# Kernel tuning notes

Measured on AMD Instinct MI355X. Metric: run time of the kernel, lower is better.

The kernel has to match this reference:

```python
import jax, jax.numpy as jnp
from jax import lax
import numpy as np

B, TQ, T = 64, 2, 2048
HID, ENC, U, FILT, K = 1024, 512, 256, 32, 31


def setup_inputs() -> dict:
    key = jax.random.key(0)
    ks = jax.random.split(key, 12)
    def w(k, shape, fan_in):
        return jax.random.normal(k, shape, jnp.float32) / np.sqrt(fan_in)
    return {
        "query": jax.random.normal(ks[0], (B, TQ, HID), jnp.float32),
        "state": jax.random.uniform(ks[1], (B, T), jnp.float32),
        "memory": jax.random.normal(ks[2], (B, T, ENC), jnp.float32),
        "Wq": w(ks[3], (HID, U), HID), "bq": jnp.zeros((U,), jnp.float32),
        "Wm": w(ks[4], (ENC, U), ENC), "bm": jnp.zeros((U,), jnp.float32),
        "Wl": w(ks[5], (FILT, U), FILT), "bl": jnp.zeros((U,), jnp.float32),
        "conv_w": w(ks[6], (FILT, 1, K), K), "conv_b": jnp.zeros((FILT,), jnp.float32),
        "We": w(ks[7], (U, U), U), "be": jnp.zeros((U,), jnp.float32),
        "v_a": w(ks[8], (U,), U),
    }


def reference(query, state, memory, Wq, bq, Wm, bm, Wl, bl, conv_w, conv_b, We, be, v_a):
    # memory projection (done in `initialize` in the original): [B,T,U]
    mem_proj = jnp.einsum("bte,eu->btu", memory, Wm) + bm
    # query projection then slice timestep 1 -> [B,1,U]
    pq = (jnp.einsum("bqh,hu->bqu", query, Wq) + bq)[:, 1:2, :]
    # location features: 1-D conv over time of previous alignment, 'same' padding
    x = state[:, None, :]                                    # [B,1,T]
    f = lax.conv_general_dilated(x, conv_w, (1,), "SAME",
                                 dimension_numbers=("NCH", "OIH", "NCH"))
    f = f + conv_b[None, :, None]                            # [B,FILT,T]
    loc = jnp.einsum("bft,fu->btu", f, Wl) + bl              # [B,T,U]
    # additive energy with tanh, reduced against v_a -> [B,T]
    h = jnp.tanh(jnp.einsum("btu,uv->btv", pq + loc + mem_proj, We) + be)
    energy = jnp.einsum("btu,u->bt", h, v_a)
    # smoothing normalization: sigmoid / sum(sigmoid)
    s = jax.nn.sigmoid(energy)
    alignment = s / jnp.sum(s, axis=-1, keepdims=True)
    # cumulate_weights=True: accumulate onto previous alignment
    cum_alignment = state + alignment
    # context against projected memory: [B,1,U]
    context = jnp.einsum("bt,btu->bu", cum_alignment, mem_proj)[:, None, :]
    return context
```

## Files before the change

### kernel.cpp

```cpp
#include <hip/hip_runtime.h>
#include <hip/hip_bf16.h>
#include <math.h>

#define Bq 64
#define Tt 2048
#define TQn 2
#define HIDn 1024
#define ENCn 512
#define Un 256
#define FILTn 32
#define KKn 31

#define TTILE 32
#define NCHUNK (Tt / TTILE)
#define LDK 520

typedef short short8 __attribute__((ext_vector_type(8)));
typedef float f32x4  __attribute__((ext_vector_type(4)));
typedef float f32x4v __attribute__((ext_vector_type(4)));
typedef unsigned short ushort_t;
typedef unsigned int   uint_t;

union S8 { short8 v; uint_t u[4]; };

__device__ __forceinline__ ushort_t f2b(float f) {
    union { float f; uint_t u; } x; x.f = f;
    uint_t r = x.u + 0x7fffu + ((x.u >> 16) & 1u);
    return (ushort_t)(r >> 16);
}
__device__ __forceinline__ uint_t cvt_pk(float lo, float hi) {
    union { __hip_bfloat162 h; uint_t u; } x;
    x.h = __float22bfloat162_rn(make_float2(lo, hi));
    return x.u;
}
__device__ __forceinline__ float b2f(uint_t u16) {
    union { uint_t i; float f; } x; x.i = u16 << 16;
    return x.f;
}
__device__ __forceinline__ float tanh_fast(float x) {
    const float e = __expf(2.0f * x);
    return 1.0f - 2.0f * __builtin_amdgcn_rcpf(e + 1.0f);
}

__device__ __forceinline__ int bp_idx(int v, int k) {
    const int seg = (k >> 5) * 16 + (v >> 6) * 4 + ((v >> 4) & 3);
    const int ln  = ((k >> 3) & 3) * 16 + (v & 15);
    return seg * 512 + ln * 8 + (k & 7);
}

__global__ void k_prep(const float* __restrict__ We, const float* __restrict__ Wm,
                       const float* __restrict__ Wl, const float* __restrict__ conv_w,
                       const float* __restrict__ bq, const float* __restrict__ bm,
                       const float* __restrict__ bl, const float* __restrict__ conv_b,
                       const float* __restrict__ query, const float* __restrict__ Wq,
                       const float* __restrict__ be,
                       ushort_t* __restrict__ Bp, ushort_t* __restrict__ CWT,
                       float* __restrict__ zconst)
{
    const int blk = blockIdx.x;
    __shared__ float wlwe[FILTn * 64];
    __shared__ float g_lds[Un];
    if (blk < 512) {
        const int v = threadIdx.x;
        const int e = blk;
        float a0 = 0.f, a1 = 0.f, a2 = 0.f, a3 = 0.f;
        #pragma unroll 4
        for (int u = 0; u < Un; u += 4) {
            a0 += Wm[(size_t)e * Un + u + 0] * We[(u + 0) * Un + v];
            a1 += Wm[(size_t)e * Un + u + 1] * We[(u + 1) * Un + v];
            a2 += Wm[(size_t)e * Un + u + 2] * We[(u + 2) * Un + v];
            a3 += Wm[(size_t)e * Un + u + 3] * We[(u + 3) * Un + v];
        }
        Bp[bp_idx(v, e)] = f2b((a0 + a1) + (a2 + a3));
    } else if (blk < 516) {
        const int vc = (blk - 512) * 64;
        for (int i = threadIdx.x; i < FILTn * 64; i += 256) {
            const int f = i >> 6, vv = i & 63;
            float a = 0.f;
            #pragma unroll 8
            for (int u = 0; u < Un; ++u) a += Wl[f * Un + u] * We[u * Un + vc + vv];
            wlwe[f * 64 + vv] = a;
        }
        __syncthreads();
        for (int i = threadIdx.x; i < 64 * 32; i += 256) {
            const int vv = i >> 5, k = i & 31;
            float a = 0.f;
            if (k < KKn) {
                #pragma unroll
                for (int f = 0; f < FILTn; ++f) a += conv_w[f * KKn + k] * wlwe[f * 64 + vv];
            }
            CWT[bp_idx(vc + vv, k)] = f2b(a);
        }
    } else {
        const int b = blk - 516;
        const int u = threadIdx.x;
        float cv = bq[u] + bm[u] + bl[u];
        #pragma unroll
        for (int f = 0; f < FILTn; ++f) cv += conv_b[f] * Wl[f * Un + u];
        const float* q = query + ((size_t)b * TQn + 1) * HIDn;
        float a0 = 0.f, a1 = 0.f, a2 = 0.f, a3 = 0.f;
        #pragma unroll 4
        for (int h = 0; h < HIDn; h += 4) {
            a0 += q[h + 0] * Wq[(size_t)(h + 0) * Un + u];
            a1 += q[h + 1] * Wq[(size_t)(h + 1) * Un + u];
            a2 += q[h + 2] * Wq[(size_t)(h + 2) * Un + u];
            a3 += q[h + 3] * Wq[(size_t)(h + 3) * Un + u];
        }
        g_lds[u] = cv + (a0 + a1) + (a2 + a3);
        __syncthreads();
        float z0 = 0.f, z1 = 0.f;
        #pragma unroll 4
        for (int uu = 0; uu < Un; uu += 2) {
            z0 += g_lds[uu]     * We[(size_t)uu * Un + u];
            z1 += g_lds[uu + 1] * We[(size_t)(uu + 1) * Un + u];
        }
        zconst[b * Un + u] = be[u] + z0 + z1;
    }
}

__global__ __launch_bounds__(256, 4) void attn_main(
    const float* __restrict__ memory, const float* __restrict__ state,
    const ushort_t* __restrict__ Bp, const ushort_t* __restrict__ CWT,
    const float* __restrict__ zconst, const float* __restrict__ v_a,
    float* __restrict__ zA, float* __restrict__ zS,
    float* __restrict__ zSsum, float* __restrict__ zStsum)
{
    const int blk = blockIdx.x;
    const int b  = blk >> 6;
    const int c  = blk & (NCHUNK - 1);
    const int t0 = c * TTILE;
    const int tid = threadIdx.x;

    __shared__ __align__(16) ushort_t mem_s[TTILE * LDK];
    __shared__ __align__(16) float sw_raw[80];
    __shared__ __align__(16) float ep_s[4][TTILE];
    __shared__ __align__(16) float s_s[TTILE];
    float* sw = sw_raw + 1;

    for (int i = tid; i < TTILE + 31; i += 256) {
        const int t = t0 - 15 + i;
        sw[i] = (t >= 0 && t < Tt) ? state[b * Tt + t] : 0.0f;
    }

    const int lane = tid & 63;
    const int w    = tid >> 6;
    const int lm   = lane & 15;
    const int lq   = lane >> 4;
    const int ncol0 = w * 64 + lm;

    const ushort_t* bp0 = Bp + (size_t)(w * 4) * 512 + lane * 8;
    const ushort_t* bp1 = bp0 + 512;
    const ushort_t* bp2 = bp0 + 1024;
    const ushort_t* bp3 = bp0 + 1536;
    const ushort_t* cp0 = CWT + (size_t)(w * 4) * 512 + lane * 8;

    short8 bbuf[2][4];
    bbuf[0][0] = *(const short8*)(bp0);
    bbuf[0][1] = *(const short8*)(bp1);
    bbuf[0][2] = *(const short8*)(bp2);
    bbuf[0][3] = *(const short8*)(bp3);
    bbuf[1][0] = *(const short8*)(bp0 + 8192);
    bbuf[1][1] = *(const short8*)(bp1 + 8192);
    bbuf[1][2] = *(const short8*)(bp2 + 8192);
    bbuf[1][3] = *(const short8*)(bp3 + 8192);

    const f32x4v* memv4 = (const f32x4v*)(memory + ((size_t)b * Tt + t0) * ENCn);
    #pragma unroll
    for (int i = 0; i < 8; ++i) {
        const int idx = i * 256 + tid;
        const int row = idx >> 6;
        const int cw8 = (idx & 63) << 3;
        const f32x4v m0 = __builtin_nontemporal_load(memv4 + 2 * idx);
        const f32x4v m1 = __builtin_nontemporal_load(memv4 + 2 * idx + 1);
        S8 v;
        v.u[0] = cvt_pk(m0.x, m0.y); v.u[1] = cvt_pk(m0.z, m0.w);
        v.u[2] = cvt_pk(m1.x, m1.y); v.u[3] = cvt_pk(m1.z, m1.w);
        *(short8*)&mem_s[row * LDK + cw8] = v.v;
    }

    f32x4 acc[2][4] = {};

    __syncthreads();

    const ushort_t* arow0 = &mem_s[(lm) * LDK + lq * 8];
    const ushort_t* arow1 = &mem_s[(16 + lm) * LDK + lq * 8];

    short8 a0c = *(const short8*)(arow0);
    short8 a1c = *(const short8*)(arow1);

    #pragma unroll
    for (int s = 0; s < 16; ++s) {
        const int sa = ((s + 1) & 15) * 32;
        const short8 a0n = *(const short8*)(arow0 + sa);
        const short8 a1n = *(const short8*)(arow1 + sa);
        acc[0][0] = __builtin_amdgcn_mfma_f32_16x16x32_bf16(a0c, bbuf[s & 1][0], acc[0][0], 0, 0, 0);
        acc[0][1] = __builtin_amdgcn_mfma_f32_16x16x32_bf16(a0c, bbuf[s & 1][1], acc[0][1], 0, 0, 0);
        acc[0][2] = __builtin_amdgcn_mfma_f32_16x16x32_bf16(a0c, bbuf[s & 1][2], acc[0][2], 0, 0, 0);
        acc[0][3] = __builtin_amdgcn_mfma_f32_16x16x32_bf16(a0c, bbuf[s & 1][3], acc[0][3], 0, 0, 0);
        acc[1][0] = __builtin_amdgcn_mfma_f32_16x16x32_bf16(a1c, bbuf[s & 1][0], acc[1][0], 0, 0, 0);
        acc[1][1] = __builtin_amdgcn_mfma_f32_16x16x32_bf16(a1c, bbuf[s & 1][1], acc[1][1], 0, 0, 0);
        acc[1][2] = __builtin_amdgcn_mfma_f32_16x16x32_bf16(a1c, bbuf[s & 1][2], acc[1][2], 0, 0, 0);
        acc[1][3] = __builtin_amdgcn_mfma_f32_16x16x32_bf16(a1c, bbuf[s & 1][3], acc[1][3], 0, 0, 0);
        const int sn = ((s + 2) & 15) * 8192;
        bbuf[s & 1][0] = *(const short8*)(bp0 + sn);
        bbuf[s & 1][1] = *(const short8*)(bp1 + sn);
        bbuf[s & 1][2] = *(const short8*)(bp2 + sn);
        bbuf[s & 1][3] = *(const short8*)(bp3 + sn);
        a0c = a0n; a1c = a1n;
    }

    {
        S8 ca0, ca1;
        #pragma unroll
        for (int j = 0; j < 4; ++j) {
            const int base0 = lm + lq * 8 + 2 * j;
            ca0.u[j] = cvt_pk(sw[base0],      sw[base0 + 1]);
            ca1.u[j] = cvt_pk(sw[base0 + 16], sw[base0 + 17]);
        }
        const short8 cb0 = *(const short8*)(cp0);
        const short8 cb1 = *(const short8*)(cp0 + 512);
        const short8 cb2 = *(const short8*)(cp0 + 1024);
        const short8 cb3 = *(const short8*)(cp0 + 1536);
        acc[0][0] = __builtin_amdgcn_mfma_f32_16x16x32_bf16(ca0.v, cb0, acc[0][0], 0, 0, 0);
        acc[0][1] = __builtin_amdgcn_mfma_f32_16x16x32_bf16(ca0.v, cb1, acc[0][1], 0, 0, 0);
        acc[0][2] = __builtin_amdgcn_mfma_f32_16x16x32_bf16(ca0.v, cb2, acc[0][2], 0, 0, 0);
        acc[0][3] = __builtin_amdgcn_mfma_f32_16x16x32_bf16(ca0.v, cb3, acc[0][3], 0, 0, 0);
        acc[1][0] = __builtin_amdgcn_mfma_f32_16x16x32_bf16(ca1.v, cb0, acc[1][0], 0, 0, 0);
        acc[1][1] = __builtin_amdgcn_mfma_f32_16x16x32_bf16(ca1.v, cb1, acc[1][1], 0, 0, 0);
        acc[1][2] = __builtin_amdgcn_mfma_f32_16x16x32_bf16(ca1.v, cb2, acc[1][2], 0, 0, 0);
        acc[1][3] = __builtin_amdgcn_mfma_f32_16x16x32_bf16(ca1.v, cb3, acc[1][3], 0, 0, 0);
    }

    float zc[4], va[4];
    #pragma unroll
    for (int nbi = 0; nbi < 4; ++nbi) {
        const int col = ncol0 + nbi * 16;
        zc[nbi] = zconst[b * Un + col];
        va[nbi] = v_a[col];
    }
    #pragma unroll
    for (int mb = 0; mb < 2; ++mb) {
        #pragma unroll
        for (int r = 0; r < 4; ++r) {
            float ep = 0.f;
            #pragma unroll
            for (int nbi = 0; nbi < 4; ++nbi)
                ep += tanh_fast(acc[mb][nbi][r] + zc[nbi]) * va[nbi];
            ep += __shfl_xor(ep, 1, 64);
            ep += __shfl_xor(ep, 2, 64);
            ep += __shfl_xor(ep, 4, 64);
            ep += __shfl_xor(ep, 8, 64);
            if (lm == 0) ep_s[w][mb * 16 + lq * 4 + r] = ep;
        }
    }
    __syncthreads();

    if (tid < 64) {
        float s = 0.f, st = 0.f;
        if (tid < TTILE) {
            const float energy = ep_s[0][tid] + ep_s[1][tid] + ep_s[2][tid] + ep_s[3][tid];
            s = __builtin_amdgcn_rcpf(1.0f + __expf(-energy));
            s_s[tid] = s;
            st = sw[15 + tid];
        }
        float ssum = s, stsum = st;
        #pragma unroll
        for (int off = 32; off >= 1; off >>= 1) {
            ssum  += __shfl_xor(ssum,  off, 64);
            stsum += __shfl_xor(stsum, off, 64);
        }
        if (tid == 0) {
            atomicAdd(&zSsum[b], ssum);
            atomicAdd(&zStsum[b], stsum);
        }
    }
    __syncthreads();

    const int e0 = tid << 1;
    float aA0 = 0.f, aA1 = 0.f, aS0 = 0.f, aS1 = 0.f;
    #pragma unroll 2
    for (int r4 = 0; r4 < TTILE / 4; ++r4) {
        const float4 sv4 = *(const float4*)&s_s[r4 * 4];
        const float4 st4 = *(const float4*)&sw[15 + r4 * 4];
        const float sv[4] = {sv4.x, sv4.y, sv4.z, sv4.w};
        const float st[4] = {st4.x, st4.y, st4.z, st4.w};
        #pragma unroll
        for (int j = 0; j < 4; ++j) {
            const int r = r4 * 4 + j;
            const uint_t mm = *(const uint_t*)&mem_s[r * LDK + e0];
            const float m0 = b2f(mm & 0xffffu);
            const float m1 = b2f(mm >> 16);
            aA0 += st[j] * m0; aA1 += st[j] * m1;
            aS0 += sv[j] * m0; aS1 += sv[j] * m1;
        }
    }
    atomicAdd(&zA[b * ENCn + e0],     aA0);
    atomicAdd(&zA[b * ENCn + e0 + 1], aA1);
    atomicAdd(&zS[b * ENCn + e0],     aS0);
    atomicAdd(&zS[b * ENCn + e0 + 1], aS1);
}

__global__ void k_final(const float* __restrict__ zA, const float* __restrict__ zS,
                        const float* __restrict__ zSsum, const float* __restrict__ zStsum,
                        const float* __restrict__ Wm, const float* __restrict__ bm,
                        float* __restrict__ out)
{
    const int b = blockIdx.x, e0 = blockIdx.y * 128, u = threadIdx.x;
    const float inv = 1.0f / zSsum[b];
    float a0 = 0.f, a1 = 0.f;
    #pragma unroll 4
    for (int e = e0; e < e0 + 128; e += 2) {
        const float c0 = zA[b * ENCn + e]     + zS[b * ENCn + e]     * inv;
        const float c1 = zA[b * ENCn + e + 1] + zS[b * ENCn + e + 1] * inv;
        a0 += c0 * Wm[(size_t)e * Un + u];
        a1 += c1 * Wm[(size_t)(e + 1) * Un + u];
    }
    float acc = a0 + a1;
    if (blockIdx.y == 0) acc += bm[u] * (zStsum[b] + 1.0f);
    atomicAdd(&out[b * Un + u], acc);
}

extern "C" void kernel_launch(void* const* d_in, const int* in_sizes, int n_in,
                              void* d_out, int out_size, void* d_ws, size_t ws_size,
                              hipStream_t stream)
{
    const float* query  = (const float*)d_in[0];
    const float* state  = (const float*)d_in[1];
    const float* memory = (const float*)d_in[2];
    const float* Wq     = (const float*)d_in[3];
    const float* bq     = (const float*)d_in[4];
    const float* Wm     = (const float*)d_in[5];
    const float* bm     = (const float*)d_in[6];
    const float* Wl     = (const float*)d_in[7];
    const float* bl     = (const float*)d_in[8];
    const float* conv_w = (const float*)d_in[9];
    const float* conv_b = (const float*)d_in[10];
    const float* We     = (const float*)d_in[11];
    const float* be     = (const float*)d_in[12];
    const float* v_a    = (const float*)d_in[13];
    float* out = (float*)d_out;

    float* ws      = (float*)d_ws;
    float* zA      = ws;
    float* zS      = ws + 32768;
    float* zSsum   = ws + 65536;
    float* zStsum  = ws + 65600;
    float* zconst  = ws + 65664;
    ushort_t* Bp    = (ushort_t*)(ws + 82048);
    ushort_t* CWT   = (ushort_t*)(ws + 147584);

    hipMemsetAsync(ws, 0, 65664 * sizeof(float), stream);
    hipMemsetAsync(out, 0, (size_t)Bq * Un * sizeof(float), stream);

    hipLaunchKernelGGL(k_prep, dim3(516 + Bq), dim3(Un), 0, stream,
                       We, Wm, Wl, conv_w, bq, bm, bl, conv_b, query, Wq, be,
                       Bp, CWT, zconst);
    hipLaunchKernelGGL(attn_main, dim3(Bq * NCHUNK), dim3(256), 0, stream,
                       memory, state, Bp, CWT, zconst, v_a, zA, zS, zSsum, zStsum);
    hipLaunchKernelGGL(k_final, dim3(Bq, 4), dim3(Un), 0, stream,
                       zA, zS, zSsum, zStsum, Wm, bm, out);
}
```

Before: 516.6 us.

## Replace per-chunk float atomics with partial buffers reduced in final kernel; triple-buffer B loads

Each attn_main block now writes its per-chunk context partial sums to a dedicated slot instead of issuing float atomicAdds onto shared per-batch accumulators. k_final first reduces the 64 chunk partials per batch through shared memory before the Wm projection. The B-fragment register prefetch in the MFMA loop goes from double to triple buffering, and those loads are moved after the memory tile staging. The aim is to remove atomic contention and shrink the memset. The cost is about 16 MB of extra partial-buffer traffic, more registers that may lower occupancy, and a heavier final kernel.

```diff
diff --git a/kernel.cpp b/kernel.cpp
--- a/kernel.cpp
+++ b/kernel.cpp
@@ -122,7 +122,7 @@
     const float* __restrict__ memory, const float* __restrict__ state,
     const ushort_t* __restrict__ Bp, const ushort_t* __restrict__ CWT,
     const float* __restrict__ zconst, const float* __restrict__ v_a,
-    float* __restrict__ zA, float* __restrict__ zS,
+    float* __restrict__ pA, float* __restrict__ pS,
     float* __restrict__ zSsum, float* __restrict__ zStsum)
 {
     const int blk = blockIdx.x;
@@ -141,28 +141,6 @@
         const int t = t0 - 15 + i;
         sw[i] = (t >= 0 && t < Tt) ? state[b * Tt + t] : 0.0f;
     }
-
-    const int lane = tid & 63;
-    const int w    = tid >> 6;
-    const int lm   = lane & 15;
-    const int lq   = lane >> 4;
-    const int ncol0 = w * 64 + lm;
-
-    const ushort_t* bp0 = Bp + (size_t)(w * 4) * 512 + lane * 8;
-    const ushort_t* bp1 = bp0 + 512;
-    const ushort_t* bp2 = bp0 + 1024;
-    const ushort_t* bp3 = bp0 + 1536;
-    const ushort_t* cp0 = CWT + (size_t)(w * 4) * 512 + lane * 8;
-
-    short8 bbuf[2][4];
-    bbuf[0][0] = *(const short8*)(bp0);
-    bbuf[0][1] = *(const short8*)(bp1);
-    bbuf[0][2] = *(const short8*)(bp2);
-    bbuf[0][3] = *(const short8*)(bp3);
-    bbuf[1][0] = *(const short8*)(bp0 + 8192);
-    bbuf[1][1] = *(const short8*)(bp1 + 8192);
-    bbuf[1][2] = *(const short8*)(bp2 + 8192);
-    bbuf[1][3] = *(const short8*)(bp3 + 8192);
 
     const f32x4v* memv4 = (const f32x4v*)(memory + ((size_t)b * Tt + t0) * ENCn);
     #pragma unroll
@@ -178,6 +156,27 @@
         *(short8*)&mem_s[row * LDK + cw8] = v.v;
     }
 
+    const int lane = tid & 63;
+    const int w    = tid >> 6;
+    const int lm   = lane & 15;
+    const int lq   = lane >> 4;
+    const int ncol0 = w * 64 + lm;
+
+    const ushort_t* bp0 = Bp + (size_t)(w * 4) * 512 + lane * 8;
+    const ushort_t* bp1 = bp0 + 512;
+    const ushort_t* bp2 = bp0 + 1024;
+    const ushort_t* bp3 = bp0 + 1536;
+    const ushort_t* cp0 = CWT + (size_t)(w * 4) * 512 + lane * 8;
+
+    short8 bbuf[3][4];
+    #pragma unroll
+    for (int d = 0; d < 3; ++d) {
+        bbuf[d][0] = *(const short8*)(bp0 + d * 8192);
+        bbuf[d][1] = *(const short8*)(bp1 + d * 8192);
+        bbuf[d][2] = *(const short8*)(bp2 + d * 8192);
+        bbuf[d][3] = *(const short8*)(bp3 + d * 8192);
+    }
+
     f32x4 acc[2][4] = {};
 
     __syncthreads();
@@ -190,22 +189,23 @@
 
     #pragma unroll
     for (int s = 0; s < 16; ++s) {
+        const int sl = s % 3;
         const int sa = ((s + 1) & 15) * 32;
         const short8 a0n = *(const short8*)(arow0 + sa);
         const short8 a1n = *(const short8*)(arow1 + sa);
-        acc[0][0] = __builtin_amdgcn_mfma_f32_16x16x32_bf16(a0c, bbuf[s & 1][0], acc[0][0], 0, 0, 0);
-        acc[0][1] = __builtin_amdgcn_mfma_f32_16x16x32_bf16(a0c, bbuf[s & 1][1], acc[0][1], 0, 0, 0);
-        acc[0][2] = __builtin_amdgcn_mfma_f32_16x16x32_bf16(a0c, bbuf[s & 1][2], acc[0][2], 0, 0, 0);
-        acc[0][3] = __builtin_amdgcn_mfma_f32_16x16x32_bf16(a0c, bbuf[s & 1][3], acc[0][3], 0, 0, 0);
-        acc[1][0] = __builtin_amdgcn_mfma_f32_16x16x32_bf16(a1c, bbuf[s & 1][0], acc[1][0], 0, 0, 0);
-        acc[1][1] = __builtin_amdgcn_mfma_f32_16x16x32_bf16(a1c, bbuf[s & 1][1], acc[1][1], 0, 0, 0);
-        acc[1][2] = __builtin_amdgcn_mfma_f32_16x16x32_bf16(a1c, bbuf[s & 1][2], acc[1][2], 0, 0, 0);
-        acc[1][3] = __builtin_amdgcn_mfma_f32_16x16x32_bf16(a1c, bbuf[s & 1][3], acc[1][3], 0, 0, 0);
-        const int sn = ((s + 2) & 15) * 8192;
-        bbuf[s & 1][0] = *(const short8*)(bp0 + sn);
-        bbuf[s & 1][1] = *(const short8*)(bp1 + sn);
-        bbuf[s & 1][2] = *(const short8*)(bp2 + sn);
-        bbuf[s & 1][3] = *(const short8*)(bp3 + sn);
+        acc[0][0] = __builtin_amdgcn_mfma_f32_16x16x32_bf16(a0c, bbuf[sl][0], acc[0][0], 0, 0, 0);
+        acc[0][1] = __builtin_amdgcn_mfma_f32_16x16x32_bf16(a0c, bbuf[sl][1], acc[0][1], 0, 0, 0);
+        acc[0][2] = __builtin_amdgcn_mfma_f32_16x16x32_bf16(a0c, bbuf[sl][2], acc[0][2], 0, 0, 0);
+        acc[0][3] = __builtin_amdgcn_mfma_f32_16x16x32_bf16(a0c, bbuf[sl][3], acc[0][3], 0, 0, 0);
+        acc[1][0] = __builtin_amdgcn_mfma_f32_16x16x32_bf16(a1c, bbuf[sl][0], acc[1][0], 0, 0, 0);
+        acc[1][1] = __builtin_amdgcn_mfma_f32_16x16x32_bf16(a1c, bbuf[sl][1], acc[1][1], 0, 0, 0);
+        acc[1][2] = __builtin_amdgcn_mfma_f32_16x16x32_bf16(a1c, bbuf[sl][2], acc[1][2], 0, 0, 0);
+        acc[1][3] = __builtin_amdgcn_mfma_f32_16x16x32_bf16(a1c, bbuf[sl][3], acc[1][3], 0, 0, 0);
+        const int sn = ((s + 3) & 15) * 8192;
+        bbuf[sl][0] = *(const short8*)(bp0 + sn);
+        bbuf[sl][1] = *(const short8*)(bp1 + sn);
+        bbuf[sl][2] = *(const short8*)(bp2 + sn);
+        bbuf[sl][3] = *(const short8*)(bp3 + sn);
         a0c = a0n; a1c = a1n;
     }
 
@@ -294,26 +294,46 @@
             aS0 += sv[j] * m0; aS1 += sv[j] * m1;
         }
     }
-    atomicAdd(&zA[b * ENCn + e0],     aA0);
-    atomicAdd(&zA[b * ENCn + e0 + 1], aA1);
-    atomicAdd(&zS[b * ENCn + e0],     aS0);
-    atomicAdd(&zS[b * ENCn + e0 + 1], aS1);
-}
-
-__global__ void k_final(const float* __restrict__ zA, const float* __restrict__ zS,
+    *(float2*)(pA + (size_t)blk * ENCn + e0) = make_float2(aA0, aA1);
+    *(float2*)(pS + (size_t)blk * ENCn + e0) = make_float2(aS0, aS1);
+}
+
+__global__ void k_final(const float* __restrict__ pA, const float* __restrict__ pS,
                         const float* __restrict__ zSsum, const float* __restrict__ zStsum,
                         const float* __restrict__ Wm, const float* __restrict__ bm,
                         float* __restrict__ out)
 {
     const int b = blockIdx.x, e0 = blockIdx.y * 128, u = threadIdx.x;
+    __shared__ float redA[256], redS[256];
+    __shared__ float zAr[128], zSr[128];
+    {
+        const int el = u & 127;
+        const int ch = (u >> 7) * 32;
+        const float* bA = pA + ((size_t)b * NCHUNK + ch) * ENCn + e0 + el;
+        const float* bS = pS + ((size_t)b * NCHUNK + ch) * ENCn + e0 + el;
+        float aA = 0.f, aS = 0.f;
+        #pragma unroll 8
+        for (int cc = 0; cc < 32; ++cc) {
+            aA += bA[(size_t)cc * ENCn];
+            aS += bS[(size_t)cc * ENCn];
+        }
+        redA[u] = aA; redS[u] = aS;
+    }
+    __syncthreads();
+    if (u < 128) {
+        zAr[u] = redA[u] + redA[u + 128];
+        zSr[u] = redS[u] + redS[u + 128];
+    }
+    __syncthreads();
+
     const float inv = 1.0f / zSsum[b];
     float a0 = 0.f, a1 = 0.f;
     #pragma unroll 4
-    for (int e = e0; e < e0 + 128; e += 2) {
-        const float c0 = zA[b * ENCn + e]     + zS[b * ENCn + e]     * inv;
-        const float c1 = zA[b * ENCn + e + 1] + zS[b * ENCn + e + 1] * inv;
-        a0 += c0 * Wm[(size_t)e * Un + u];
-        a1 += c1 * Wm[(size_t)(e + 1) * Un + u];
+    for (int i = 0; i < 128; i += 2) {
+        const float c0 = zAr[i]     + zSr[i]     * inv;
+        const float c1 = zAr[i + 1] + zSr[i + 1] * inv;
+        a0 += c0 * Wm[(size_t)(e0 + i) * Un + u];
+        a1 += c1 * Wm[(size_t)(e0 + i + 1) * Un + u];
     }
     float acc = a0 + a1;
     if (blockIdx.y == 0) acc += bm[u] * (zStsum[b] + 1.0f);
@@ -341,22 +361,22 @@
     float* out = (float*)d_out;
 
     float* ws      = (float*)d_ws;
-    float* zA      = ws;
-    float* zS      = ws + 32768;
-    float* zSsum   = ws + 65536;
-    float* zStsum  = ws + 65600;
-    float* zconst  = ws + 65664;
-    ushort_t* Bp    = (ushort_t*)(ws + 82048);
-    ushort_t* CWT   = (ushort_t*)(ws + 147584);
-
-    hipMemsetAsync(ws, 0, 65664 * sizeof(float), stream);
+    float* zSsum   = ws;
+    float* zStsum  = ws + 64;
+    float* zconst  = ws + 128;
+    float* pA      = ws + 16512;
+    float* pS      = ws + 2113664;
+    ushort_t* Bp    = (ushort_t*)(ws + 4210816);
+    ushort_t* CWT   = (ushort_t*)(ws + 4276352);
+
+    hipMemsetAsync(ws, 0, 128 * sizeof(float), stream);
     hipMemsetAsync(out, 0, (size_t)Bq * Un * sizeof(float), stream);
 
     hipLaunchKernelGGL(k_prep, dim3(516 + Bq), dim3(Un), 0, stream,
                        We, Wm, Wl, conv_w, bq, bm, bl, conv_b, query, Wq, be,
                        Bp, CWT, zconst);
     hipLaunchKernelGGL(attn_main, dim3(Bq * NCHUNK), dim3(256), 0, stream,
-                       memory, state, Bp, CWT, zconst, v_a, zA, zS, zSsum, zStsum);
+                       memory, state, Bp, CWT, zconst, v_a, pA, pS, zSsum, zStsum);
     hipLaunchKernelGGL(k_final, dim3(Bq, 4), dim3(Un), 0, stream,
-                       zA, zS, zSsum, zStsum, Wm, bm, out);
-}
+                       pA, pS, zSsum, zStsum, Wm, bm, out);
+}
```

After: 505.7 us. 1.02x faster.
